# Performance work log

Measured on AMD Instinct MI355X. Metric: run time of the kernel, lower is better.

Reference implementation:

```python
import jax, jax.numpy as jnp
import numpy as np

N, D, H, E, TOP_K = 4096, 1024, 2048, 8, 2


def setup_inputs() -> dict:
    key = jax.random.key(0)
    ks = jax.random.split(key, 8)
    s = 0.02
    return {
        "x": jax.random.normal(ks[0], (N, D), dtype=jnp.float32),
        "gate_W": jax.random.normal(ks[1], (D, E), dtype=jnp.float32) * s,
        "gate_b": jnp.zeros((E,), dtype=jnp.float32),
        "W1": jax.random.normal(ks[2], (E, D, H), dtype=jnp.float32) * s,
        "b1": jnp.zeros((E, H), dtype=jnp.float32),
        "W2": jax.random.normal(ks[3], (E, H, D), dtype=jnp.float32) * s,
        "b2": jnp.zeros((E, D), dtype=jnp.float32),
    }


def reference(x, gate_W, gate_b, W1, b1, W2, b2):
    # TopKGate: softmax over expert logits, pick top-k probs + indices.
    logits = x @ gate_W + gate_b                    # [N, E]
    probs = jax.nn.softmax(logits, axis=-1)
    gates, idxs = jax.lax.top_k(probs, TOP_K)        # [N, K] each

    # Combine weights w[n, e] = sum_k gates[n,k] * (idxs[n,k] == e).
    onehot = jax.nn.one_hot(idxs, E, dtype=x.dtype)  # [N, K, E]
    w = jnp.einsum("nke,nk->ne", onehot, gates)      # [N, E]

    # Dense per-expert MLP on all tokens; unrouted tokens get weight 0,
    # so the math matches the masked gather/scatter original exactly.
    h = jax.nn.relu(jnp.einsum("nd,edh->enh", x, W1) + b1[:, None, :])  # [E,N,H]
    y = jnp.einsum("enh,ehd->end", h, W2) + b2[:, None, :]               # [E,N,D]
    out = jnp.einsum("end,ne->nd", y, w)                                 # [N,D]
    return out
```

## Files before the change

kernel.cpp:

```cpp
#include <hip/hip_runtime.h>
#include <hip/hip_bf16.h>
#include <cstdint>

#define N_TOK 4096
#define DIM   1024
#define HID   2048
#define NE    8

typedef __bf16 bf16x8 __attribute__((ext_vector_type(8)));
typedef __bf16 bf16x4 __attribute__((ext_vector_type(4)));
typedef float  f32x4  __attribute__((ext_vector_type(4)));

__device__ __forceinline__ void gload16(const void* g, void* l) {
    __builtin_amdgcn_global_load_lds(
        (const __attribute__((address_space(1))) void*)g,
        (__attribute__((address_space(3))) void*)l, 16, 0, 0);
}

__global__ void transpose_cvt_all(const float* __restrict__ W1, const float* __restrict__ W2,
                                  __bf16* __restrict__ w1t, __bf16* __restrict__ w2t) {
    int lin = blockIdx.x;
    const float* src; __bf16* dst; int R, C, rx, cy;
    if (lin < 16384) {
        const int e = lin >> 11, rem = lin & 2047;
        rx = rem >> 6; cy = rem & 63;
        R = DIM; C = HID;
        src = W1 + (size_t)e * DIM * HID; dst = w1t + (size_t)e * DIM * HID;
    } else {
        lin -= 16384;
        const int e = lin >> 11, rem = lin & 2047;
        rx = rem >> 5; cy = rem & 31;
        R = HID; C = DIM;
        src = W2 + (size_t)e * DIM * HID; dst = w2t + (size_t)e * DIM * HID;
    }
    __shared__ float t[32][33];
    const int r0 = rx * 32, c0 = cy * 32;
    const int tr = threadIdx.x >> 3;
    const int tc = (threadIdx.x & 7) * 4;
    float4 v = *(const float4*)&src[(size_t)(r0 + tr) * C + c0 + tc];
    t[tr][tc + 0] = v.x; t[tr][tc + 1] = v.y; t[tr][tc + 2] = v.z; t[tr][tc + 3] = v.w;
    __syncthreads();
    bf16x4 o;
    o[0] = (__bf16)t[tc + 0][tr];
    o[1] = (__bf16)t[tc + 1][tr];
    o[2] = (__bf16)t[tc + 2][tr];
    o[3] = (__bf16)t[tc + 3][tr];
    *(bf16x4*)&dst[(size_t)(c0 + tr) * R + r0 + tc] = o;
}

__global__ void gate_kernel(const float* __restrict__ x, const float* __restrict__ gW,
                            const float* __restrict__ gb, int* __restrict__ top_idx,
                            float* __restrict__ top_gate, __bf16* __restrict__ xb) {
    const int tokn = blockIdx.x * 4 + (threadIdx.x >> 6);
    const int lane = threadIdx.x & 63;
    const float4* xr = (const float4*)(x + (size_t)tokn * DIM);
    __bf16* xbr = xb + (size_t)tokn * DIM;
    float acc[NE] = {};
#pragma unroll
    for (int i = 0; i < 4; i++) {
        const int v4 = i * 64 + lane;
        const float4 xv = xr[v4];
        bf16x4 xc = { (__bf16)xv.x, (__bf16)xv.y, (__bf16)xv.z, (__bf16)xv.w };
        *(bf16x4*)&xbr[v4 * 4] = xc;
        const float* wb = &gW[v4 * 4 * NE];
        const float xs[4] = { xv.x, xv.y, xv.z, xv.w };
#pragma unroll
        for (int j = 0; j < 4; j++) {
            const float4 wa = *(const float4*)&wb[j * NE];
            const float4 wc = *(const float4*)&wb[j * NE + 4];
            acc[0] += xs[j] * wa.x; acc[1] += xs[j] * wa.y;
            acc[2] += xs[j] * wa.z; acc[3] += xs[j] * wa.w;
            acc[4] += xs[j] * wc.x; acc[5] += xs[j] * wc.y;
            acc[6] += xs[j] * wc.z; acc[7] += xs[j] * wc.w;
        }
    }
#pragma unroll
    for (int e = 0; e < NE; e++)
#pragma unroll
        for (int s = 32; s > 0; s >>= 1)
            acc[e] += __shfl_down(acc[e], s, 64);
    if (lane == 0) {
        float lg[NE], p[NE];
        float mx = -1e30f;
#pragma unroll
        for (int e = 0; e < NE; e++) { lg[e] = acc[e] + gb[e]; mx = fmaxf(mx, lg[e]); }
        float s = 0.f;
#pragma unroll
        for (int e = 0; e < NE; e++) { p[e] = __expf(lg[e] - mx); s += p[e]; }
        const float inv = 1.f / s;
#pragma unroll
        for (int e = 0; e < NE; e++) p[e] *= inv;
        int i0 = 0; float p0 = p[0];
#pragma unroll
        for (int e = 1; e < NE; e++) if (p[e] > p0) { p0 = p[e]; i0 = e; }
        int i1 = -1; float p1 = -1.f;
#pragma unroll
        for (int e = 0; e < NE; e++) if (e != i0 && p[e] > p1) { p1 = p[e]; i1 = e; }
        top_idx[tokn * 2] = i0;  top_idx[tokn * 2 + 1] = i1;
        top_gate[tokn * 2] = p0; top_gate[tokn * 2 + 1] = p1;
    }
}

__global__ void count_kernel(const int* __restrict__ top_idx, int* __restrict__ cnt) {
    __shared__ int hist[NE];
    if (threadIdx.x < NE) hist[threadIdx.x] = 0;
    __syncthreads();
    const int n = blockIdx.x * 256 + threadIdx.x;
    atomicAdd(&hist[top_idx[n * 2]], 1);
    atomicAdd(&hist[top_idx[n * 2 + 1]], 1);
    __syncthreads();
    if (threadIdx.x < NE) atomicAdd(&cnt[threadIdx.x], hist[threadIdx.x]);
}

__global__ void build_kernel(const int* __restrict__ top_idx, const int* __restrict__ cnt,
                             int* __restrict__ run, int* __restrict__ row_token,
                             int* __restrict__ tok_row) {
    __shared__ int soffs[NE];
    __shared__ int lrun[NE];
    __shared__ int base[NE];
    if (threadIdx.x == 0) {
        int s = 0;
        for (int e = 0; e < NE; e++) { soffs[e] = s; s += cnt[e]; }
    }
    if (threadIdx.x < NE) lrun[threadIdx.x] = 0;
    __syncthreads();
    const int n = blockIdx.x * 256 + threadIdx.x;
    const int e0 = top_idx[n * 2], e1 = top_idx[n * 2 + 1];
    const int p0 = atomicAdd(&lrun[e0], 1);
    const int p1 = atomicAdd(&lrun[e1], 1);
    __syncthreads();
    if (threadIdx.x < NE) base[threadIdx.x] = atomicAdd(&run[threadIdx.x], lrun[threadIdx.x]);
    __syncthreads();
    const int r0 = soffs[e0] + base[e0] + p0;
    const int r1 = soffs[e1] + base[e1] + p1;
    row_token[r0] = n; tok_row[n * 2] = r0;
    row_token[r1] = n; tok_row[n * 2 + 1] = r1;
}

__global__ __launch_bounds__(256, 2) void gemm1_kernel(
    const __bf16* __restrict__ xb, const __bf16* __restrict__ w1t,
    const float* __restrict__ b1, const int* __restrict__ cnt,
    const int* __restrict__ row_token, __bf16* __restrict__ h) {
    const int lin = blockIdx.x;
    const int e   = lin & 7;
    const int t   = lin >> 3;
    const int n0  = (t & 7) * 256;
    const int mt  = t >> 3;
    int off_e = 0;
    for (int i = 0; i < e; i++) off_e += cnt[i];
    const int ce = cnt[e];
    if (mt * 128 >= ce) return;

    __shared__ __bf16 lA[8192];
    __shared__ __bf16 lB[16384];

    const int tid  = threadIdx.x;
    const int lane = tid & 63;
    const int wid  = tid >> 6;
    const int quad = lane >> 4;
    const int l16  = lane & 15;
    const int wm   = wid & 1;
    const int wn   = wid >> 1;

    const int lrow = lane >> 3;
    const int cch  = (lane & 7) ^ lrow;
    const __bf16* aros[4]; char* ldsA[4];
#pragma unroll
    for (int j = 0; j < 4; j++) {
        const int g   = wid * 4 + j;
        const int row = g * 8 + lrow;
        int gr = off_e + mt * 128 + row;
        gr = gr < 2 * N_TOK - 1 ? gr : 2 * N_TOK - 1;
        const int tok = row_token[gr] & (N_TOK - 1);
        aros[j] = xb + (size_t)tok * DIM + cch * 8;
        ldsA[j] = (char*)lA + g * 1024;
    }
    const __bf16* bros[8]; char* ldsB[8];
#pragma unroll
    for (int j = 0; j < 8; j++) {
        const int g   = wid * 8 + j;
        const int row = g * 8 + lrow;
        bros[j] = w1t + ((size_t)e * HID + n0 + row) * DIM + cch * 8;
        ldsB[j] = (char*)lB + g * 1024;
    }

    f32x4 acc[4][8] = {};

    for (int kk = 0; kk < DIM; kk += 64) {
#pragma unroll
        for (int j = 0; j < 4; j++) gload16(aros[j] + kk, ldsA[j]);
#pragma unroll
        for (int j = 0; j < 8; j++) gload16(bros[j] + kk, ldsB[j]);
        __syncthreads();
#pragma unroll
        for (int hh = 0; hh < 2; hh++) {
            const int sw = (((hh * 4 + quad) ^ (l16 & 7)) << 4);
            bf16x8 af[4], bfr[8];
#pragma unroll
            for (int mi = 0; mi < 4; mi++)
                af[mi] = *(const bf16x8*)((const char*)lA + (wm * 64 + mi * 16 + l16) * 128 + sw);
#pragma unroll
            for (int ni = 0; ni < 8; ni++)
                bfr[ni] = *(const bf16x8*)((const char*)lB + (wn * 128 + ni * 16 + l16) * 128 + sw);
#pragma unroll
            for (int mi = 0; mi < 4; mi++)
#pragma unroll
                for (int ni = 0; ni < 8; ni++)
                    acc[mi][ni] = __builtin_amdgcn_mfma_f32_16x16x32_bf16(af[mi], bfr[ni], acc[mi][ni], 0, 0, 0);
        }
        __syncthreads();
    }

#pragma unroll
    for (int ni = 0; ni < 8; ni++) {
        const int col = n0 + wn * 128 + ni * 16 + l16;
        const float bias = b1[e * HID + col];
#pragma unroll
        for (int mi = 0; mi < 4; mi++) {
#pragma unroll
            for (int r = 0; r < 4; r++) {
                const int lr = wm * 64 + mi * 16 + quad * 4 + r;
                const int gm = mt * 128 + lr;
                if (gm < ce) {
                    float v = acc[mi][ni][r] + bias;
                    v = v > 0.f ? v : 0.f;
                    h[(size_t)(off_e + gm) * HID + col] = (__bf16)v;
                }
            }
        }
    }
}

__global__ __launch_bounds__(256, 2) void gemm2_kernel(
    const __bf16* __restrict__ h, const __bf16* __restrict__ w2t,
    const float* __restrict__ b2, const int* __restrict__ cnt,
    float* __restrict__ y) {
    const int lin = blockIdx.x;
    const int e   = lin & 7;
    const int t   = lin >> 3;
    const int n0  = (t & 7) * 128;
    const int mt  = t >> 3;
    int off_e = 0;
    for (int i = 0; i < e; i++) off_e += cnt[i];
    const int ce = cnt[e];
    if (mt * 128 >= ce) return;

    __shared__ __bf16 lA[8192];
    __shared__ __bf16 lB[8192];

    const int tid  = threadIdx.x;
    const int lane = tid & 63;
    const int wid  = tid >> 6;
    const int quad = lane >> 4;
    const int l16  = lane & 15;
    const int wm   = wid & 1;
    const int wn   = wid >> 1;

    const int lrow = lane >> 3;
    const int cch  = (lane & 7) ^ lrow;
    const __bf16* aros[4]; const __bf16* bros[4];
    char* ldsA[4]; char* ldsB[4];
#pragma unroll
    for (int j = 0; j < 4; j++) {
        const int row = (wid * 4 + j) * 8 + lrow;
        int gr = off_e + mt * 128 + row;
        gr = gr < 2 * N_TOK - 1 ? gr : 2 * N_TOK - 1;
        aros[j] = h   + (size_t)gr * HID + cch * 8;
        bros[j] = w2t + ((size_t)e * DIM + n0 + row) * HID + cch * 8;
        ldsA[j] = (char*)lA + (wid * 4 + j) * 1024;
        ldsB[j] = (char*)lB + (wid * 4 + j) * 1024;
    }

    f32x4 acc[4][4] = {};

    for (int kk = 0; kk < HID; kk += 64) {
#pragma unroll
        for (int j = 0; j < 4; j++) gload16(aros[j] + kk, ldsA[j]);
#pragma unroll
        for (int j = 0; j < 4; j++) gload16(bros[j] + kk, ldsB[j]);
        __syncthreads();
#pragma unroll
        for (int hh = 0; hh < 2; hh++) {
            const int sw = (((hh * 4 + quad) ^ (l16 & 7)) << 4);
            bf16x8 af[4], bfr[4];
#pragma unroll
            for (int mi = 0; mi < 4; mi++)
                af[mi] = *(const bf16x8*)((const char*)lA + (wm * 64 + mi * 16 + l16) * 128 + sw);
#pragma unroll
            for (int ni = 0; ni < 4; ni++)
                bfr[ni] = *(const bf16x8*)((const char*)lB + (wn * 64 + ni * 16 + l16) * 128 + sw);
#pragma unroll
            for (int mi = 0; mi < 4; mi++)
#pragma unroll
                for (int ni = 0; ni < 4; ni++)
                    acc[mi][ni] = __builtin_amdgcn_mfma_f32_16x16x32_bf16(af[mi], bfr[ni], acc[mi][ni], 0, 0, 0);
        }
        __syncthreads();
    }

#pragma unroll
    for (int mi = 0; mi < 4; mi++) {
#pragma unroll
        for (int r = 0; r < 4; r++) {
            const int lr = wm * 64 + mi * 16 + quad * 4 + r;
            const int gm = mt * 128 + lr;
            if (gm < ce) {
#pragma unroll
                for (int ni = 0; ni < 4; ni++) {
                    const int col = n0 + wn * 64 + ni * 16 + l16;
                    y[(size_t)(off_e + gm) * DIM + col] = acc[mi][ni][r] + b2[e * DIM + col];
                }
            }
        }
    }
}

__global__ void combine_kernel(const float* __restrict__ y, const int* __restrict__ tok_row,
                               const float* __restrict__ top_gate, float* __restrict__ out) {
    const int n = blockIdx.x;
    const int d = threadIdx.x * 4;
    const int r0 = tok_row[n * 2], r1 = tok_row[n * 2 + 1];
    const float g0 = top_gate[n * 2], g1 = top_gate[n * 2 + 1];
    float4 a = *(const float4*)&y[(size_t)r0 * DIM + d];
    float4 b = *(const float4*)&y[(size_t)r1 * DIM + d];
    float4 o = { g0 * a.x + g1 * b.x, g0 * a.y + g1 * b.y,
                 g0 * a.z + g1 * b.z, g0 * a.w + g1 * b.w };
    *(float4*)&out[(size_t)n * DIM + d] = o;
}

extern "C" void kernel_launch(void* const* d_in, const int* in_sizes, int n_in,
                              void* d_out, int out_size, void* d_ws, size_t ws_size,
                              hipStream_t stream) {
    const float* x  = (const float*)d_in[0];
    const float* gW = (const float*)d_in[1];
    const float* gb = (const float*)d_in[2];
    const float* W1 = (const float*)d_in[3];
    const float* b1 = (const float*)d_in[4];
    const float* W2 = (const float*)d_in[5];
    const float* b2 = (const float*)d_in[6];
    float* out = (float*)d_out;

    char* ws = (char*)d_ws;
    __bf16* xb   = (__bf16*)(ws);
    __bf16* w1t  = (__bf16*)(ws + ((size_t)8  << 20));
    float*  ybuf = (float*) (ws + ((size_t)8  << 20));
    __bf16* w2t  = (__bf16*)(ws + ((size_t)40 << 20));
    __bf16* hbuf = (__bf16*)(ws + ((size_t)72 << 20));
    char* tail   = ws + ((size_t)104 << 20);
    int*   row_token = (int*)(tail);
    int*   tok_row   = (int*)(tail + 32768);
    int*   top_idx   = (int*)(tail + 65536);
    float* top_gate  = (float*)(tail + 98304);
    int*   cnt       = (int*)(tail + 131072);
    int*   run       = cnt + 32;

    hipMemsetAsync(cnt, 0, 256, stream);

    gate_kernel<<<N_TOK / 4, 256, 0, stream>>>(x, gW, gb, top_idx, top_gate, xb);
    count_kernel<<<N_TOK / 256, 256, 0, stream>>>(top_idx, cnt);
    build_kernel<<<N_TOK / 256, 256, 0, stream>>>(top_idx, cnt, run, row_token, tok_row);
    transpose_cvt_all<<<32768, 256, 0, stream>>>(W1, W2, w1t, w2t);
    gemm1_kernel<<<NE * 32 * (HID / 256), 256, 0, stream>>>(xb, w1t, b1, cnt, row_token, hbuf);
    gemm2_kernel<<<NE * 32 * (DIM / 128), 256, 0, stream>>>(hbuf, w2t, b2, cnt, ybuf);
    combine_kernel<<<N_TOK, 256, 0, stream>>>(ybuf, tok_row, top_gate, out);
}
```

Baseline: 337.9 us.

## Enlarge transpose tiles, shrink gemm1 tiles, reorder block mapping, store y in bf16

The weight transpose now uses 64x64 tiles with 16-byte bf16 stores and a quarter of the blocks, which cuts launch overhead and widens the writes. gemm1 drops from 128x256 to 128x128 tiles, which lowers register and LDS use and doubles the block count. Both GEMMs now map blocks M-tile-major so blocks sharing a weight N-slice run close together. The intermediate y is stored as bf16 instead of fp32 to halve combine traffic, at the cost of extra rounding error in the output.

```diff
diff --git a/kernel.cpp b/kernel.cpp
--- a/kernel.cpp
+++ b/kernel.cpp
@@ -17,35 +17,50 @@
         (__attribute__((address_space(3))) void*)l, 16, 0, 0);
 }
 
-__global__ void transpose_cvt_all(const float* __restrict__ W1, const float* __restrict__ W2,
-                                  __bf16* __restrict__ w1t, __bf16* __restrict__ w2t) {
+__global__ __launch_bounds__(256) void transpose_cvt_all(
+    const float* __restrict__ W1, const float* __restrict__ W2,
+    __bf16* __restrict__ w1t, __bf16* __restrict__ w2t) {
     int lin = blockIdx.x;
     const float* src; __bf16* dst; int R, C, rx, cy;
-    if (lin < 16384) {
-        const int e = lin >> 11, rem = lin & 2047;
-        rx = rem >> 6; cy = rem & 63;
+    if (lin < 4096) {
+        const int e = lin >> 9, rem = lin & 511;
+        rx = rem >> 5; cy = rem & 31;
         R = DIM; C = HID;
         src = W1 + (size_t)e * DIM * HID; dst = w1t + (size_t)e * DIM * HID;
     } else {
-        lin -= 16384;
-        const int e = lin >> 11, rem = lin & 2047;
-        rx = rem >> 5; cy = rem & 31;
+        lin -= 4096;
+        const int e = lin >> 9, rem = lin & 511;
+        rx = rem >> 4; cy = rem & 15;
         R = HID; C = DIM;
         src = W2 + (size_t)e * DIM * HID; dst = w2t + (size_t)e * DIM * HID;
     }
-    __shared__ float t[32][33];
-    const int r0 = rx * 32, c0 = cy * 32;
-    const int tr = threadIdx.x >> 3;
-    const int tc = (threadIdx.x & 7) * 4;
-    float4 v = *(const float4*)&src[(size_t)(r0 + tr) * C + c0 + tc];
-    t[tr][tc + 0] = v.x; t[tr][tc + 1] = v.y; t[tr][tc + 2] = v.z; t[tr][tc + 3] = v.w;
-    __syncthreads();
-    bf16x4 o;
-    o[0] = (__bf16)t[tc + 0][tr];
-    o[1] = (__bf16)t[tc + 1][tr];
-    o[2] = (__bf16)t[tc + 2][tr];
-    o[3] = (__bf16)t[tc + 3][tr];
-    *(bf16x4*)&dst[(size_t)(c0 + tr) * R + r0 + tc] = o;
+    __shared__ float t[64][65];
+    const int r0 = rx * 64, c0 = cy * 64;
+    const int tid = threadIdx.x;
+    {
+        const int tr = tid >> 2;
+        const int tc = (tid & 3) * 16;
+        const float* s = &src[(size_t)(r0 + tr) * C + c0 + tc];
+#pragma unroll
+        for (int j = 0; j < 4; j++) {
+            float4 v = *(const float4*)(s + 4 * j);
+            t[tr][tc + 4 * j + 0] = v.x; t[tr][tc + 4 * j + 1] = v.y;
+            t[tr][tc + 4 * j + 2] = v.z; t[tr][tc + 4 * j + 3] = v.w;
+        }
+    }
+    __syncthreads();
+    {
+        const int cidx = tid >> 2;
+        const int seg  = tid & 3;
+        bf16x8 o0, o1;
+#pragma unroll
+        for (int i = 0; i < 8; i++) o0[i] = (__bf16)t[seg * 16 + i][cidx];
+#pragma unroll
+        for (int i = 0; i < 8; i++) o1[i] = (__bf16)t[seg * 16 + 8 + i][cidx];
+        __bf16* d = &dst[(size_t)(c0 + cidx) * R + r0 + seg * 16];
+        *(bf16x8*)(d)     = o0;
+        *(bf16x8*)(d + 8) = o1;
+    }
 }
 
 __global__ void gate_kernel(const float* __restrict__ x, const float* __restrict__ gW,
@@ -144,15 +159,15 @@
     const int lin = blockIdx.x;
     const int e   = lin & 7;
     const int t   = lin >> 3;
-    const int n0  = (t & 7) * 256;
-    const int mt  = t >> 3;
+    const int mt  = t & 31;
+    const int n0  = (t >> 5) * 128;
     int off_e = 0;
     for (int i = 0; i < e; i++) off_e += cnt[i];
     const int ce = cnt[e];
     if (mt * 128 >= ce) return;
 
     __shared__ __bf16 lA[8192];
-    __shared__ __bf16 lB[16384];
+    __shared__ __bf16 lB[8192];
 
     const int tid  = threadIdx.x;
     const int lane = tid & 63;
@@ -164,56 +179,50 @@
 
     const int lrow = lane >> 3;
     const int cch  = (lane & 7) ^ lrow;
-    const __bf16* aros[4]; char* ldsA[4];
+    const __bf16* aros[4]; const __bf16* bros[4];
+    char* ldsA[4]; char* ldsB[4];
 #pragma unroll
     for (int j = 0; j < 4; j++) {
-        const int g   = wid * 4 + j;
-        const int row = g * 8 + lrow;
+        const int row = (wid * 4 + j) * 8 + lrow;
         int gr = off_e + mt * 128 + row;
         gr = gr < 2 * N_TOK - 1 ? gr : 2 * N_TOK - 1;
         const int tok = row_token[gr] & (N_TOK - 1);
-        aros[j] = xb + (size_t)tok * DIM + cch * 8;
-        ldsA[j] = (char*)lA + g * 1024;
-    }
-    const __bf16* bros[8]; char* ldsB[8];
-#pragma unroll
-    for (int j = 0; j < 8; j++) {
-        const int g   = wid * 8 + j;
-        const int row = g * 8 + lrow;
+        aros[j] = xb  + (size_t)tok * DIM + cch * 8;
         bros[j] = w1t + ((size_t)e * HID + n0 + row) * DIM + cch * 8;
-        ldsB[j] = (char*)lB + g * 1024;
-    }
-
-    f32x4 acc[4][8] = {};
+        ldsA[j] = (char*)lA + (wid * 4 + j) * 1024;
+        ldsB[j] = (char*)lB + (wid * 4 + j) * 1024;
+    }
+
+    f32x4 acc[4][4] = {};
 
     for (int kk = 0; kk < DIM; kk += 64) {
 #pragma unroll
         for (int j = 0; j < 4; j++) gload16(aros[j] + kk, ldsA[j]);
 #pragma unroll
-        for (int j = 0; j < 8; j++) gload16(bros[j] + kk, ldsB[j]);
+        for (int j = 0; j < 4; j++) gload16(bros[j] + kk, ldsB[j]);
         __syncthreads();
 #pragma unroll
         for (int hh = 0; hh < 2; hh++) {
             const int sw = (((hh * 4 + quad) ^ (l16 & 7)) << 4);
-            bf16x8 af[4], bfr[8];
+            bf16x8 af[4], bfr[4];
 #pragma unroll
             for (int mi = 0; mi < 4; mi++)
                 af[mi] = *(const bf16x8*)((const char*)lA + (wm * 64 + mi * 16 + l16) * 128 + sw);
 #pragma unroll
-            for (int ni = 0; ni < 8; ni++)
-                bfr[ni] = *(const bf16x8*)((const char*)lB + (wn * 128 + ni * 16 + l16) * 128 + sw);
+            for (int ni = 0; ni < 4; ni++)
+                bfr[ni] = *(const bf16x8*)((const char*)lB + (wn * 64 + ni * 16 + l16) * 128 + sw);
 #pragma unroll
             for (int mi = 0; mi < 4; mi++)
 #pragma unroll
-                for (int ni = 0; ni < 8; ni++)
+                for (int ni = 0; ni < 4; ni++)
                     acc[mi][ni] = __builtin_amdgcn_mfma_f32_16x16x32_bf16(af[mi], bfr[ni], acc[mi][ni], 0, 0, 0);
         }
         __syncthreads();
     }
 
 #pragma unroll
-    for (int ni = 0; ni < 8; ni++) {
-        const int col = n0 + wn * 128 + ni * 16 + l16;
+    for (int ni = 0; ni < 4; ni++) {
+        const int col = n0 + wn * 64 + ni * 16 + l16;
         const float bias = b1[e * HID + col];
 #pragma unroll
         for (int mi = 0; mi < 4; mi++) {
@@ -234,12 +243,12 @@
 __global__ __launch_bounds__(256, 2) void gemm2_kernel(
     const __bf16* __restrict__ h, const __bf16* __restrict__ w2t,
     const float* __restrict__ b2, const int* __restrict__ cnt,
-    float* __restrict__ y) {
+    __bf16* __restrict__ y) {
     const int lin = blockIdx.x;
     const int e   = lin & 7;
     const int t   = lin >> 3;
-    const int n0  = (t & 7) * 128;
-    const int mt  = t >> 3;
+    const int mt  = t & 31;
+    const int n0  = (t >> 5) * 128;
     int off_e = 0;
     for (int i = 0; i < e; i++) off_e += cnt[i];
     const int ce = cnt[e];
@@ -308,23 +317,23 @@
 #pragma unroll
                 for (int ni = 0; ni < 4; ni++) {
                     const int col = n0 + wn * 64 + ni * 16 + l16;
-                    y[(size_t)(off_e + gm) * DIM + col] = acc[mi][ni][r] + b2[e * DIM + col];
+                    y[(size_t)(off_e + gm) * DIM + col] = (__bf16)(acc[mi][ni][r] + b2[e * DIM + col]);
                 }
             }
         }
     }
 }
 
-__global__ void combine_kernel(const float* __restrict__ y, const int* __restrict__ tok_row,
+__global__ void combine_kernel(const __bf16* __restrict__ y, const int* __restrict__ tok_row,
                                const float* __restrict__ top_gate, float* __restrict__ out) {
     const int n = blockIdx.x;
     const int d = threadIdx.x * 4;
     const int r0 = tok_row[n * 2], r1 = tok_row[n * 2 + 1];
     const float g0 = top_gate[n * 2], g1 = top_gate[n * 2 + 1];
-    float4 a = *(const float4*)&y[(size_t)r0 * DIM + d];
-    float4 b = *(const float4*)&y[(size_t)r1 * DIM + d];
-    float4 o = { g0 * a.x + g1 * b.x, g0 * a.y + g1 * b.y,
-                 g0 * a.z + g1 * b.z, g0 * a.w + g1 * b.w };
+    bf16x4 a = *(const bf16x4*)&y[(size_t)r0 * DIM + d];
+    bf16x4 b = *(const bf16x4*)&y[(size_t)r1 * DIM + d];
+    float4 o = { g0 * (float)a[0] + g1 * (float)b[0], g0 * (float)a[1] + g1 * (float)b[1],
+                 g0 * (float)a[2] + g1 * (float)b[2], g0 * (float)a[3] + g1 * (float)b[3] };
     *(float4*)&out[(size_t)n * DIM + d] = o;
 }
 
@@ -343,7 +352,7 @@
     char* ws = (char*)d_ws;
     __bf16* xb   = (__bf16*)(ws);
     __bf16* w1t  = (__bf16*)(ws + ((size_t)8  << 20));
-    float*  ybuf = (float*) (ws + ((size_t)8  << 20));
+    __bf16* ybuf = (__bf16*)(ws + ((size_t)8  << 20));
     __bf16* w2t  = (__bf16*)(ws + ((size_t)40 << 20));
     __bf16* hbuf = (__bf16*)(ws + ((size_t)72 << 20));
     char* tail   = ws + ((size_t)104 << 20);
@@ -359,8 +368,8 @@
     gate_kernel<<<N_TOK / 4, 256, 0, stream>>>(x, gW, gb, top_idx, top_gate, xb);
     count_kernel<<<N_TOK / 256, 256, 0, stream>>>(top_idx, cnt);
     build_kernel<<<N_TOK / 256, 256, 0, stream>>>(top_idx, cnt, run, row_token, tok_row);
-    transpose_cvt_all<<<32768, 256, 0, stream>>>(W1, W2, w1t, w2t);
-    gemm1_kernel<<<NE * 32 * (HID / 256), 256, 0, stream>>>(xb, w1t, b1, cnt, row_token, hbuf);
+    transpose_cvt_all<<<8192, 256, 0, stream>>>(W1, W2, w1t, w2t);
+    gemm1_kernel<<<NE * 32 * (HID / 128), 256, 0, stream>>>(xb, w1t, b1, cnt, row_token, hbuf);
     gemm2_kernel<<<NE * 32 * (DIM / 128), 256, 0, stream>>>(hbuf, w2t, b2, cnt, ybuf);
     combine_kernel<<<N_TOK, 256, 0, stream>>>(ybuf, tok_row, top_gate, out);
 }
```

After: 313.0 us. 7.4% less time.
